# Performance work log

Measured on AMD Instinct MI355X. Metric: run time of the kernel, lower is better.

## Reference

```python
import jax, jax.numpy as jnp
import numpy as np

D_IN = 384
HID = 384
D_OUT = 384

def _kaiming(key, fan_in, fan_out):
    return jax.random.normal(key, (fan_in, fan_out), dtype=jnp.float32) * np.sqrt(2.0 / fan_in)

def setup_inputs() -> dict:
    key = jax.random.key(0)
    ks = jax.random.split(key, 12)
    B, O, T = 8, 1024, 8192
    obj_vecs = jax.random.normal(ks[0], (B, O, D_IN), dtype=jnp.float32)
    pred_vecs = jax.random.normal(ks[1], (B, T, D_IN), dtype=jnp.float32)
    edges = jax.random.randint(ks[2], (B, T, 2), 0, O, dtype=jnp.int64)
    # gconv1: [3D -> H -> 2H + Dout]; gconv2: [H -> H -> Dout]
    w1a = _kaiming(ks[3], 3 * D_IN, HID); b1a = jnp.zeros((HID,), jnp.float32)
    w1b = _kaiming(ks[4], HID, 2 * HID + D_OUT); b1b = jnp.zeros((2 * HID + D_OUT,), jnp.float32)
    w2a = _kaiming(ks[5], HID, HID); b2a = jnp.zeros((HID,), jnp.float32)
    w2b = _kaiming(ks[6], HID, D_OUT); b2b = jnp.zeros((D_OUT,), jnp.float32)
    return {"obj_vecs": obj_vecs, "pred_vecs": pred_vecs, "edges": edges,
            "w1a": w1a, "b1a": b1a, "w1b": w1b, "b1b": b1b,
            "w2a": w2a, "b2a": b2a, "w2b": w2b, "b2b": b2b}

def _gconv_forward(obj_vecs, pred_vecs, edges, w1a, b1a, w1b, b1b, w2a, b2a, w2b, b2b):
    B, O, D = obj_vecs.shape
    s_idx = edges[:, :, 0]  # (B, T)
    o_idx = edges[:, :, 1]
    batch = jnp.arange(B)[:, None]
    subj = obj_vecs[batch, s_idx]  # (B, T, D) gather
    objt = obj_vecs[batch, o_idx]
    triple = jnp.concatenate([subj, pred_vecs, objt], axis=-1)  # (B, T, 3D)
    h = jax.nn.relu(triple @ w1a + b1a)
    t = jax.nn.relu(h @ w1b + b1b)  # (B, T, 2H + Dout)
    new_s = t[:, :, :HID]
    new_p = t[:, :, HID:HID + D_OUT]
    new_o = t[:, :, HID + D_OUT:]
    # scatter_add per batch into (O, H) buffers
    def agg(si, oi, vs, vo):
        return jnp.zeros((O, HID), vs.dtype).at[si].add(vs).at[oi].add(vo)
    pooled = jax.vmap(agg)(s_idx, o_idx, new_s, new_o)  # (B, O, H)
    pooled = pooled / jnp.linalg.norm(pooled)  # global Frobenius norm, as in torch .norm()
    out_obj = jax.nn.relu(jax.nn.relu(pooled @ w2a + b2a) @ w2b + b2b)
    return out_obj, new_p

def reference(obj_vecs, pred_vecs, edges, w1a, b1a, w1b, b1b, w2a, b2a, w2b, b2b):
    return _gconv_forward(obj_vecs, pred_vecs, edges, w1a, b1a, w1b, b1b, w2a, b2a, w2b, b2b)
```

## Files before the change

kernel.cpp:

```cpp
#include <hip/hip_runtime.h>
#include <hip/hip_bf16.h>

#define NB 8
#define NT 8192
#define NO 1024
#define DD 384
#define K1 1152
#define M1 65536
#define MO 8192

typedef __attribute__((ext_vector_type(8))) short bf16x8;
typedef __attribute__((ext_vector_type(4))) float f32x4;
typedef __attribute__((ext_vector_type(4))) unsigned short u16x4;

__device__ __forceinline__ unsigned short f2bf(float f) {
    union { float f; unsigned u; } v; v.f = f;
    unsigned r = v.u + 0x7FFFu + ((v.u >> 16) & 1u);
    return (unsigned short)(r >> 16);
}
__device__ __forceinline__ float bf2f(unsigned short h) {
    union { unsigned u; float f; } v; v.u = ((unsigned)h) << 16;
    return v.f;
}
__device__ __forceinline__ bf16x8 pack8(f32x4 a, f32x4 b) {
    bf16x8 r;
    r[0] = (short)f2bf(a[0]); r[1] = (short)f2bf(a[1]);
    r[2] = (short)f2bf(a[2]); r[3] = (short)f2bf(a[3]);
    r[4] = (short)f2bf(b[0]); r[5] = (short)f2bf(b[1]);
    r[6] = (short)f2bf(b[2]); r[7] = (short)f2bf(b[3]);
    return r;
}
__device__ __forceinline__ void gload16(const void* g, void* l) {
    __builtin_amdgcn_global_load_lds(
        (const __attribute__((address_space(1))) unsigned int*)g,
        (__attribute__((address_space(3))) unsigned int*)l, 16, 0, 0);
}

__global__ void k_cvt4(const float* __restrict__ s, unsigned short* __restrict__ d, int n) {
    int i = (blockIdx.x * blockDim.x + threadIdx.x) * 4;
    if (i >= n) return;
    f32x4 v = *(const f32x4*)(s + i);
    u16x4 o;
    o[0] = f2bf(v[0]); o[1] = f2bf(v[1]); o[2] = f2bf(v[2]); o[3] = f2bf(v[3]);
    *(u16x4*)(d + i) = o;
}
__global__ void k_tr(const float* __restrict__ s, unsigned short* __restrict__ d, int K, int N) {
    int k = blockIdx.x;
    int n = blockIdx.y * blockDim.x + threadIdx.x;
    if (n < N) d[n * K + k] = f2bf(s[k * N + n]);
}

__global__ void k_ss1(const float* __restrict__ p, float* __restrict__ partial, int n4) {
    __shared__ float wsum[4];
    int stride = gridDim.x * blockDim.x;
    float s = 0.f;
    for (int i = blockIdx.x * blockDim.x + threadIdx.x; i < n4; i += stride) {
        f32x4 v = *(const f32x4*)(p + i * 4);
        s += v[0] * v[0] + v[1] * v[1] + v[2] * v[2] + v[3] * v[3];
    }
#pragma unroll
    for (int off = 32; off; off >>= 1) s += __shfl_down(s, off, 64);
    if ((threadIdx.x & 63) == 0) wsum[threadIdx.x >> 6] = s;
    __syncthreads();
    if (threadIdx.x == 0)
        partial[blockIdx.x] = wsum[0] + wsum[1] + wsum[2] + wsum[3];
}
__global__ void k_ss2(const float* __restrict__ partial, float* __restrict__ o) {
    float s = partial[threadIdx.x];
#pragma unroll
    for (int off = 32; off; off >>= 1) s += __shfl_down(s, off, 64);
    __shared__ float w0, w1;
    if (threadIdx.x == 0) w0 = s;
    if (threadIdx.x == 64) w1 = s;
    __syncthreads();
    if (threadIdx.x == 0) o[0] = w0 + w1;
}
__global__ void k_normcvt(const float* __restrict__ p, const float* __restrict__ ss,
                          unsigned short* __restrict__ o) {
    int i = (blockIdx.x * blockDim.x + threadIdx.x) * 8;
    float s = rsqrtf(ss[0]);
    f32x4 a = *(const f32x4*)(p + i), b = *(const f32x4*)(p + i + 4);
    a *= s; b *= s;
    *(bf16x8*)(o + i) = pack8(a, b);
}

__global__ void k_hist(const int* __restrict__ edges, int* __restrict__ cnt) {
    int i = blockIdx.x * 256 + threadIdx.x;
    int2 e = *(const int2*)&edges[(size_t)i * 2];
    int b = i >> 13;
    atomicAdd(&cnt[(b << 10) + e.x], 1);
    atomicAdd(&cnt[(b << 10) + e.y], 1);
}
__global__ void k_scan(const int* __restrict__ cnt, int* __restrict__ offs) {
    __shared__ int a[1024];
    int b = blockIdx.x, t = threadIdx.x;
    int own = cnt[(b << 10) + t];
    a[t] = own;
    __syncthreads();
    for (int s = 1; s < 1024; s <<= 1) {
        int v = (t >= s) ? a[t - s] : 0;
        __syncthreads();
        a[t] += v;
        __syncthreads();
    }
    offs[(b << 10) + t] = a[t] - own;
}
__global__ void k_fill(const int* __restrict__ edges, const int* __restrict__ offs,
                       int* __restrict__ cur, int* __restrict__ elist) {
    int i = blockIdx.x * 256 + threadIdx.x;
    int2 e = *(const int2*)&edges[(size_t)i * 2];
    int b = i >> 13, t = i & (NT - 1);
    int ps = atomicAdd(&cur[(b << 10) + e.x], 1);
    elist[(b << 14) + offs[(b << 10) + e.x] + ps] = t * 2;
    int po = atomicAdd(&cur[(b << 10) + e.y], 1);
    elist[(b << 14) + offs[(b << 10) + e.y] + po] = t * 2 + 1;
}
__global__ void k_pool(const unsigned short* __restrict__ sob, const int* __restrict__ cnt,
                       const int* __restrict__ offs, const int* __restrict__ elist,
                       float* __restrict__ pooled) {
    int w = (blockIdx.x * 256 + threadIdx.x) >> 6;
    int lane = threadIdx.x & 63;
    if (lane >= 48) return;
    int b = w >> 10, o = w & (NO - 1);
    int len = cnt[(b << 10) + o];
    const int* lst = elist + (b << 14) + offs[(b << 10) + o];
    f32x4 a0 = {0.f, 0.f, 0.f, 0.f}, a1 = {0.f, 0.f, 0.f, 0.f};
    f32x4 c0 = {0.f, 0.f, 0.f, 0.f}, c1 = {0.f, 0.f, 0.f, 0.f};
    int j = 0;
    for (; j + 1 < len; j += 2) {
        int e0 = lst[j], e1 = lst[j + 1];
        bf16x8 v0 = *(const bf16x8*)(sob + ((size_t)((b << 13) + (e0 >> 1))) * 768 + (e0 & 1) * DD + lane * 8);
        bf16x8 v1 = *(const bf16x8*)(sob + ((size_t)((b << 13) + (e1 >> 1))) * 768 + (e1 & 1) * DD + lane * 8);
        a0[0] += bf2f((unsigned short)v0[0]); a0[1] += bf2f((unsigned short)v0[1]);
        a0[2] += bf2f((unsigned short)v0[2]); a0[3] += bf2f((unsigned short)v0[3]);
        a1[0] += bf2f((unsigned short)v0[4]); a1[1] += bf2f((unsigned short)v0[5]);
        a1[2] += bf2f((unsigned short)v0[6]); a1[3] += bf2f((unsigned short)v0[7]);
        c0[0] += bf2f((unsigned short)v1[0]); c0[1] += bf2f((unsigned short)v1[1]);
        c0[2] += bf2f((unsigned short)v1[2]); c0[3] += bf2f((unsigned short)v1[3]);
        c1[0] += bf2f((unsigned short)v1[4]); c1[1] += bf2f((unsigned short)v1[5]);
        c1[2] += bf2f((unsigned short)v1[6]); c1[3] += bf2f((unsigned short)v1[7]);
    }
    if (j < len) {
        int e0 = lst[j];
        bf16x8 v0 = *(const bf16x8*)(sob + ((size_t)((b << 13) + (e0 >> 1))) * 768 + (e0 & 1) * DD + lane * 8);
        a0[0] += bf2f((unsigned short)v0[0]); a0[1] += bf2f((unsigned short)v0[1]);
        a0[2] += bf2f((unsigned short)v0[2]); a0[3] += bf2f((unsigned short)v0[3]);
        a1[0] += bf2f((unsigned short)v0[4]); a1[1] += bf2f((unsigned short)v0[5]);
        a1[2] += bf2f((unsigned short)v0[6]); a1[3] += bf2f((unsigned short)v0[7]);
    }
    a0 += c0; a1 += c1;
    float* dst = pooled + ((size_t)((b << 10) + o)) * DD + lane * 8;
    *(f32x4*)dst = a0;
    *(f32x4*)(dst + 4) = a1;
}

__launch_bounds__(512, 1)
__global__ void gemm_g1(const unsigned short* __restrict__ objb,
                        const float* __restrict__ predf,
                        const int* __restrict__ edges,
                        const unsigned short* __restrict__ Bt,
                        const float* __restrict__ bias,
                        unsigned short* __restrict__ outb)
{
    const int tid = threadIdx.x;
    const int lane = tid & 63;
    const int d = blockIdx.x;
    const int bid = (d & 7) * 64 + (d >> 3);
    const int m0 = bid * 128;

    __shared__ unsigned short lds[2][32768];

    const int rb = tid >> 3;
    const int c8 = ((tid & 7) ^ (rb & 7)) * 8;

    const int bb = (m0 >> 13) << 10;
    int er0[2], er1[2];
#pragma unroll
    for (int i = 0; i < 2; ++i) {
        int2 e = *(const int2*)&edges[(size_t)(m0 + i * 64 + rb) * 2];
        er0[i] = bb + e.x;
        er1[i] = bb + e.y;
    }

    f32x4 acc[4][6];
#pragma unroll
    for (int i = 0; i < 4; ++i)
#pragma unroll
        for (int j = 0; j < 6; ++j) acc[i][j] = (f32x4){0.f, 0.f, 0.f, 0.f};

    const int wid = tid >> 6, wm = wid >> 2, wn = wid & 3;
    const int l16 = lane & 15, lg = lane >> 4;

#pragma unroll
    for (int i = 0; i < 2; ++i)
        gload16(objb + (size_t)er0[i] * DD + c8, &lds[0][i * 4096 + tid * 8]);
#pragma unroll
    for (int i = 0; i < 6; ++i)
        gload16(Bt + (size_t)(i * 64 + rb) * K1 + c8, &lds[0][8192 + i * 4096 + tid * 8]);

    const int nsteps = K1 / 64;
    for (int t = 0; t < nsteps; ++t) {
        const int cur = t & 1;
        const int tn = t + 1;
        if (tn < nsteps) {
            const int nseg = tn / 6;
            const int ko = (tn - nseg * 6) * 64;
            if (nseg == 1) {
                f32x4 pf[2][2];
#pragma unroll
                for (int i = 0; i < 2; ++i) {
                    const float* p = predf + (size_t)(m0 + i * 64 + rb) * DD + ko + c8;
                    pf[i][0] = *(const f32x4*)p;
                    pf[i][1] = *(const f32x4*)(p + 4);
                }
#pragma unroll
                for (int i = 0; i < 6; ++i)
                    gload16(Bt + (size_t)(i * 64 + rb) * K1 + tn * 64 + c8,
                            &lds[cur ^ 1][8192 + i * 4096 + tid * 8]);
#pragma unroll
                for (int i = 0; i < 2; ++i)
                    *(bf16x8*)(&lds[cur ^ 1][i * 4096 + tid * 8]) = pack8(pf[i][0], pf[i][1]);
            } else {
                const unsigned short* asrc0 = (nseg == 0) ? objb + (size_t)er0[0] * DD + ko + c8
                                                          : objb + (size_t)er1[0] * DD + ko + c8;
                const unsigned short* asrc1 = (nseg == 0) ? objb + (size_t)er0[1] * DD + ko + c8
                                                          : objb + (size_t)er1[1] * DD + ko + c8;
                gload16(asrc0, &lds[cur ^ 1][0 * 4096 + tid * 8]);
                gload16(asrc1, &lds[cur ^ 1][1 * 4096 + tid * 8]);
#pragma unroll
                for (int i = 0; i < 6; ++i)
                    gload16(Bt + (size_t)(i * 64 + rb) * K1 + tn * 64 + c8,
                            &lds[cur ^ 1][8192 + i * 4096 + tid * 8]);
                asm volatile("s_waitcnt vmcnt(8)" ::: "memory");
            }
        } else {
            asm volatile("s_waitcnt vmcnt(0)" ::: "memory");
        }
        __builtin_amdgcn_s_barrier();
        const unsigned short* At = &lds[cur][0];
        const unsigned short* Bl = &lds[cur][8192];
#pragma unroll
        for (int kt = 0; kt < 2; ++kt) {
            const int cs = ((kt * 4 + lg) ^ (l16 & 7)) * 8;
            bf16x8 af[4], bfr[6];
#pragma unroll
            for (int mt = 0; mt < 4; ++mt)
                af[mt] = *(const bf16x8*)(At + (wm * 64 + mt * 16 + l16) * 64 + cs);
#pragma unroll
            for (int nn = 0; nn < 6; ++nn)
                bfr[nn] = *(const bf16x8*)(Bl + (wn * 96 + nn * 16 + l16) * 64 + cs);
#pragma unroll
            for (int mt = 0; mt < 4; ++mt)
#pragma unroll
                for (int nn = 0; nn < 6; ++nn)
                    acc[mt][nn] = __builtin_amdgcn_mfma_f32_16x16x32_bf16(af[mt], bfr[nn], acc[mt][nn], 0, 0, 0);
        }
        asm volatile("s_waitcnt lgkmcnt(0)" ::: "memory");
        __builtin_amdgcn_s_barrier();
    }

#pragma unroll
    for (int nn = 0; nn < 6; ++nn) {
        int gn = wn * 96 + nn * 16 + l16;
        float bv = bias[gn];
#pragma unroll
        for (int mt = 0; mt < 4; ++mt) {
            int rbase = wm * 64 + mt * 16 + lg * 4;
#pragma unroll
            for (int rg = 0; rg < 4; ++rg) {
                int gr = m0 + rbase + rg;
                float v = fmaxf(acc[mt][nn][rg] + bv, 0.0f);
                outb[(size_t)gr * DD + gn] = f2bf(v);
            }
        }
    }
}

template <int EPI, int YFOLD>
__launch_bounds__(512, 1)
__global__ void gemm_p(const unsigned short* __restrict__ Abf,
                       const unsigned short* __restrict__ Bt,
                       const float* __restrict__ bias,
                       unsigned short* __restrict__ outb,
                       float* __restrict__ outf,
                       int K, int ldC, int bt0p, int btys, int cstride)
{
    const int tid = threadIdx.x;
    const int lane = tid & 63;
    const int d = blockIdx.x;
    const int chunk = gridDim.x >> 3;
    const int bid = (d & 7) * chunk + (d >> 3);
    int xb, y;
    if (YFOLD) { y = bid & 1; xb = bid >> 1; }
    else       { y = 0;       xb = bid;      }
    const int m0 = xb * 128;
    const int bt0 = bt0p + y * btys;
    const int col0 = y * cstride;

    __shared__ unsigned short lds[2][32768];

    const int rb = tid >> 3;
    const int c8 = ((tid & 7) ^ (rb & 7)) * 8;

    f32x4 acc[4][6];
#pragma unroll
    for (int i = 0; i < 4; ++i)
#pragma unroll
        for (int j = 0; j < 6; ++j) acc[i][j] = (f32x4){0.f, 0.f, 0.f, 0.f};

    const int wid = tid >> 6, wm = wid >> 2, wn = wid & 3;
    const int l16 = lane & 15, lg = lane >> 4;

#define STAGE_P(BUF, KK)                                                                   \
    {                                                                                      \
        _Pragma("unroll")                                                                  \
        for (int i = 0; i < 6; ++i)                                                        \
            gload16(Bt + (size_t)(bt0 + i * 64 + rb) * K + (KK) + c8,                      \
                    &lds[BUF][8192 + i * 4096 + tid * 8]);                                 \
        _Pragma("unroll")                                                                  \
        for (int i = 0; i < 2; ++i)                                                        \
            gload16(Abf + (size_t)(m0 + i * 64 + rb) * K + (KK) + c8,                      \
                    &lds[BUF][i * 4096 + tid * 8]);                                        \
    }

    const int nt = K / 64;
    STAGE_P(0, 0)
    for (int t = 0; t < nt; ++t) {
        const int cur = t & 1;
        if (t + 1 < nt) {
            STAGE_P(cur ^ 1, (t + 1) * 64)
            asm volatile("s_waitcnt vmcnt(8)" ::: "memory");
        } else {
            asm volatile("s_waitcnt vmcnt(0)" ::: "memory");
        }
        __builtin_amdgcn_s_barrier();
        const unsigned short* At = &lds[cur][0];
        const unsigned short* Bl = &lds[cur][8192];
#pragma unroll
        for (int kt = 0; kt < 2; ++kt) {
            const int cs = ((kt * 4 + lg) ^ (l16 & 7)) * 8;
            bf16x8 af[4], bfr[6];
#pragma unroll
            for (int mt = 0; mt < 4; ++mt)
                af[mt] = *(const bf16x8*)(At + (wm * 64 + mt * 16 + l16) * 64 + cs);
#pragma unroll
            for (int nn = 0; nn < 6; ++nn)
                bfr[nn] = *(const bf16x8*)(Bl + (wn * 96 + nn * 16 + l16) * 64 + cs);
#pragma unroll
            for (int mt = 0; mt < 4; ++mt)
#pragma unroll
                for (int nn = 0; nn < 6; ++nn)
                    acc[mt][nn] = __builtin_amdgcn_mfma_f32_16x16x32_bf16(af[mt], bfr[nn], acc[mt][nn], 0, 0, 0);
        }
        asm volatile("s_waitcnt lgkmcnt(0)" ::: "memory");
        __builtin_amdgcn_s_barrier();
    }
#undef STAGE_P

#pragma unroll
    for (int nn = 0; nn < 6; ++nn) {
        int gn = wn * 96 + nn * 16 + l16;
        float bv = bias[bt0 + gn];
#pragma unroll
        for (int mt = 0; mt < 4; ++mt) {
            int rbase = wm * 64 + mt * 16 + lg * 4;
#pragma unroll
            for (int rg = 0; rg < 4; ++rg) {
                int gr = m0 + rbase + rg;
                float v = fmaxf(acc[mt][nn][rg] + bv, 0.0f);
                if (EPI == 0) outb[(size_t)gr * ldC + col0 + gn] = f2bf(v);
                else          outf[(size_t)gr * ldC + col0 + gn] = v;
            }
        }
    }
}

extern "C" void kernel_launch(void* const* d_in, const int* in_sizes, int n_in,
                              void* d_out, int out_size, void* d_ws, size_t ws_size,
                              hipStream_t stream)
{
    const float* obj  = (const float*)d_in[0];
    const float* pred = (const float*)d_in[1];
    const int* edges  = (const int*)d_in[2];
    const float* w1a  = (const float*)d_in[3];
    const float* b1a  = (const float*)d_in[4];
    const float* w1b  = (const float*)d_in[5];
    const float* b1b  = (const float*)d_in[6];
    const float* w2a  = (const float*)d_in[7];
    const float* b2a  = (const float*)d_in[8];
    const float* w2b  = (const float*)d_in[9];
    const float* b2b  = (const float*)d_in[10];

    float* out_obj = (float*)d_out;
    float* newp    = out_obj + (size_t)MO * DD;
    unsigned short* sob = (unsigned short*)newp;

    unsigned short* objb = (unsigned short*)d_ws;
    unsigned short* w1aT = objb + (size_t)NB * NO * DD;
    unsigned short* w1bT = w1aT + (size_t)DD * K1;
    unsigned short* w2aT = w1bT + (size_t)K1 * DD;
    unsigned short* w2bT = w2aT + (size_t)DD * DD;
    unsigned short* hbuf = w2bT + (size_t)DD * DD;
    float* pooled = (float*)(hbuf + (size_t)M1 * DD);
    float* sumsq  = pooled + (size_t)MO * DD;
    unsigned short* hid2 = (unsigned short*)(sumsq + 4);
    int* cnt   = (int*)(hid2 + (size_t)MO * DD);
    int* cur   = cnt + NB * NO;
    int* offs  = cur + NB * NO;
    int* elist = offs + NB * NO;
    float* partial = (float*)(elist + 2 * M1);
    unsigned short* poolb = objb;

    hipLaunchKernelGGL(k_cvt4, dim3(3072), dim3(256), 0, stream, obj, objb, NB * NO * DD);
    hipLaunchKernelGGL(k_tr, dim3(K1, 3), dim3(128), 0, stream, w1a, w1aT, K1, DD);
    hipLaunchKernelGGL(k_tr, dim3(DD, 9), dim3(128), 0, stream, w1b, w1bT, DD, K1);
    hipLaunchKernelGGL(k_tr, dim3(DD, 3), dim3(128), 0, stream, w2a, w2aT, DD, DD);
    hipLaunchKernelGGL(k_tr, dim3(DD, 3), dim3(128), 0, stream, w2b, w2bT, DD, DD);
    hipMemsetAsync(cnt, 0, 2 * NB * NO * sizeof(int), stream);

    hipLaunchKernelGGL(gemm_g1, dim3(M1 / 128), dim3(512), 0, stream,
                       objb, pred, edges, w1aT, b1a, hbuf);

    hipLaunchKernelGGL((gemm_p<0, 1>), dim3(2 * M1 / 128), dim3(512), 0, stream,
                       hbuf, w1bT, b1b, sob, (float*)nullptr, DD, 2 * DD, 0, 2 * DD, DD);

    hipLaunchKernelGGL(k_hist, dim3(256), dim3(256), 0, stream, edges, cnt);
    hipLaunchKernelGGL(k_scan, dim3(8), dim3(1024), 0, stream, cnt, offs);
    hipLaunchKernelGGL(k_fill, dim3(256), dim3(256), 0, stream, edges, offs, cur, elist);
    hipLaunchKernelGGL(k_pool, dim3(2048), dim3(256), 0, stream, sob, cnt, offs, elist, pooled);

    hipLaunchKernelGGL((gemm_p<2, 0>), dim3(M1 / 128), dim3(512), 0, stream,
                       hbuf, w1bT, b1b, (unsigned short*)nullptr, newp, DD, DD, DD, 0, 0);

    hipLaunchKernelGGL(k_ss1, dim3(128), dim3(256), 0, stream, pooled, partial, MO * DD / 4);
    hipLaunchKernelGGL(k_ss2, dim3(1), dim3(128), 0, stream, partial, sumsq);
    hipLaunchKernelGGL(k_normcvt, dim3(1536), dim3(256), 0, stream, pooled, sumsq, poolb);

    hipLaunchKernelGGL((gemm_p<0, 0>), dim3(MO / 128), dim3(512), 0, stream,
                       poolb, w2aT, b2a, hid2, (float*)nullptr, DD, DD, 0, 0, 0);

    hipLaunchKernelGGL((gemm_p<2, 0>), dim3(MO / 128), dim3(512), 0, stream,
                       hid2, w2bT, b2b, (unsigned short*)nullptr, out_obj, DD, DD, 0, 0, 0);
}
```

Measured before the change: 270.0 us.

## Pre-pack GEMM operands into tiled swizzled images for contiguous LDS loads

Weights and intermediate activations (hidden buffer, normalized pooled, hid2) are written directly in a per-k-tile, per-row-block swizzled image layout that matches the LDS layout. Each GEMM stage can then fetch a fully contiguous 64 KB chunk per tile with global_load_lds instead of strided row loads. Producer epilogues now do scattered 2-byte stores into the image layout, and the weight packing kernel reads with strided access.

Result: slower. 302.6 us (+12.1%).

```diff
diff --git a/kernel.cpp b/kernel.cpp
--- a/kernel.cpp
+++ b/kernel.cpp
@@ -35,6 +35,10 @@
         (const __attribute__((address_space(1))) unsigned int*)g,
         (__attribute__((address_space(3))) unsigned int*)l, 16, 0, 0);
 }
+__device__ __forceinline__ size_t aimg_off(int kt, int nblk, int blk, int r, int kc) {
+    return ((size_t)(kt * nblk + blk)) * 8192 + (size_t)((r >> 6) * 4096)
+         + (size_t)(((r & 63) * 8 + ((kc >> 3) ^ (r & 7))) * 8) + (kc & 7);
+}
 
 __global__ void k_cvt4(const float* __restrict__ s, unsigned short* __restrict__ d, int n) {
     int i = (blockIdx.x * blockDim.x + threadIdx.x) * 4;
@@ -44,10 +48,23 @@
     o[0] = f2bf(v[0]); o[1] = f2bf(v[1]); o[2] = f2bf(v[2]); o[3] = f2bf(v[3]);
     *(u16x4*)(d + i) = o;
 }
-__global__ void k_tr(const float* __restrict__ s, unsigned short* __restrict__ d, int K, int N) {
-    int k = blockIdx.x;
-    int n = blockIdx.y * blockDim.x + threadIdx.x;
-    if (n < N) d[n * K + k] = f2bf(s[k * N + n]);
+__global__ void k_pack(const float* __restrict__ src, unsigned short* __restrict__ dst,
+                       int Nsrc, int ntiles) {
+    const int tid = threadIdx.x;
+    const int kt = blockIdx.x, panel = blockIdx.y;
+    const int rb = tid >> 3;
+    const int c8 = ((tid & 7) ^ (rb & 7)) * 8;
+    const int base_row = panel * 384;
+    unsigned short* d = dst + ((size_t)(panel * ntiles + kt)) * 24576 + tid * 8;
+#pragma unroll
+    for (int i = 0; i < 6; ++i) {
+        int row = base_row + i * 64 + rb;
+        bf16x8 v;
+#pragma unroll
+        for (int j = 0; j < 8; ++j)
+            v[j] = (short)f2bf(src[(size_t)(kt * 64 + c8 + j) * Nsrc + row]);
+        *(bf16x8*)(d + i * 4096) = v;
+    }
 }
 
 __global__ void k_ss1(const float* __restrict__ p, float* __restrict__ partial, int n4) {
@@ -76,12 +93,14 @@
     if (threadIdx.x == 0) o[0] = w0 + w1;
 }
 __global__ void k_normcvt(const float* __restrict__ p, const float* __restrict__ ss,
-                          unsigned short* __restrict__ o) {
-    int i = (blockIdx.x * blockDim.x + threadIdx.x) * 8;
+                          unsigned short* __restrict__ oimg) {
+    int u = blockIdx.x * 256 + threadIdx.x;
+    int m = u / 48, k0 = (u - m * 48) * 8;
     float s = rsqrtf(ss[0]);
-    f32x4 a = *(const f32x4*)(p + i), b = *(const f32x4*)(p + i + 4);
+    f32x4 a = *(const f32x4*)(p + (size_t)m * DD + k0);
+    f32x4 b = *(const f32x4*)(p + (size_t)m * DD + k0 + 4);
     a *= s; b *= s;
-    *(bf16x8*)(o + i) = pack8(a, b);
+    *(bf16x8*)(oimg + aimg_off(k0 >> 6, 64, m >> 7, m & 127, k0 & 63)) = pack8(a, b);
 }
 
 __global__ void k_hist(const int* __restrict__ edges, int* __restrict__ cnt) {
@@ -158,9 +177,9 @@
 __global__ void gemm_g1(const unsigned short* __restrict__ objb,
                         const float* __restrict__ predf,
                         const int* __restrict__ edges,
-                        const unsigned short* __restrict__ Bt,
+                        const unsigned short* __restrict__ Bimg,
                         const float* __restrict__ bias,
-                        unsigned short* __restrict__ outb)
+                        unsigned short* __restrict__ outimg)
 {
     const int tid = threadIdx.x;
     const int lane = tid & 63;
@@ -196,7 +215,7 @@
         gload16(objb + (size_t)er0[i] * DD + c8, &lds[0][i * 4096 + tid * 8]);
 #pragma unroll
     for (int i = 0; i < 6; ++i)
-        gload16(Bt + (size_t)(i * 64 + rb) * K1 + c8, &lds[0][8192 + i * 4096 + tid * 8]);
+        gload16(Bimg + i * 4096 + tid * 8, &lds[0][8192 + i * 4096 + tid * 8]);
 
     const int nsteps = K1 / 64;
     for (int t = 0; t < nsteps; ++t) {
@@ -215,7 +234,7 @@
                 }
 #pragma unroll
                 for (int i = 0; i < 6; ++i)
-                    gload16(Bt + (size_t)(i * 64 + rb) * K1 + tn * 64 + c8,
+                    gload16(Bimg + (size_t)tn * 24576 + i * 4096 + tid * 8,
                             &lds[cur ^ 1][8192 + i * 4096 + tid * 8]);
 #pragma unroll
                 for (int i = 0; i < 2; ++i)
@@ -229,7 +248,7 @@
                 gload16(asrc1, &lds[cur ^ 1][1 * 4096 + tid * 8]);
 #pragma unroll
                 for (int i = 0; i < 6; ++i)
-                    gload16(Bt + (size_t)(i * 64 + rb) * K1 + tn * 64 + c8,
+                    gload16(Bimg + (size_t)tn * 24576 + i * 4096 + tid * 8,
                             &lds[cur ^ 1][8192 + i * 4096 + tid * 8]);
                 asm volatile("s_waitcnt vmcnt(8)" ::: "memory");
             }
@@ -270,7 +289,7 @@
             for (int rg = 0; rg < 4; ++rg) {
                 int gr = m0 + rbase + rg;
                 float v = fmaxf(acc[mt][nn][rg] + bv, 0.0f);
-                outb[(size_t)gr * DD + gn] = f2bf(v);
+                outimg[aimg_off(gn >> 6, 512, gr >> 7, gr & 127, gn & 63)] = f2bf(v);
             }
         }
     }
@@ -278,12 +297,13 @@
 
 template <int EPI, int YFOLD>
 __launch_bounds__(512, 1)
-__global__ void gemm_p(const unsigned short* __restrict__ Abf,
-                       const unsigned short* __restrict__ Bt,
+__global__ void gemm_p(const unsigned short* __restrict__ Aimg,
+                       const unsigned short* __restrict__ Bimg,
                        const float* __restrict__ bias,
                        unsigned short* __restrict__ outb,
                        float* __restrict__ outf,
-                       int K, int ldC, int bt0p, int btys, int cstride)
+                       int ntile, int anblk, int onblk, int ldC,
+                       int bt0p, int btys, int cstride, int bimg_y_off)
 {
     const int tid = threadIdx.x;
     const int lane = tid & 63;
@@ -296,11 +316,9 @@
     const int m0 = xb * 128;
     const int bt0 = bt0p + y * btys;
     const int col0 = y * cstride;
+    const unsigned short* Bp = Bimg + (size_t)y * bimg_y_off;
 
     __shared__ unsigned short lds[2][32768];
-
-    const int rb = tid >> 3;
-    const int c8 = ((tid & 7) ^ (rb & 7)) * 8;
 
     f32x4 acc[4][6];
 #pragma unroll
@@ -311,24 +329,23 @@
     const int wid = tid >> 6, wm = wid >> 2, wn = wid & 3;
     const int l16 = lane & 15, lg = lane >> 4;
 
-#define STAGE_P(BUF, KK)                                                                   \
+#define STAGE_P(BUF, T)                                                                    \
     {                                                                                      \
         _Pragma("unroll")                                                                  \
         for (int i = 0; i < 6; ++i)                                                        \
-            gload16(Bt + (size_t)(bt0 + i * 64 + rb) * K + (KK) + c8,                      \
+            gload16(Bp + (size_t)(T) * 24576 + i * 4096 + tid * 8,                         \
                     &lds[BUF][8192 + i * 4096 + tid * 8]);                                 \
         _Pragma("unroll")                                                                  \
         for (int i = 0; i < 2; ++i)                                                        \
-            gload16(Abf + (size_t)(m0 + i * 64 + rb) * K + (KK) + c8,                      \
+            gload16(Aimg + ((size_t)((T) * anblk + xb)) * 8192 + i * 4096 + tid * 8,       \
                     &lds[BUF][i * 4096 + tid * 8]);                                        \
     }
 
-    const int nt = K / 64;
     STAGE_P(0, 0)
-    for (int t = 0; t < nt; ++t) {
+    for (int t = 0; t < ntile; ++t) {
         const int cur = t & 1;
-        if (t + 1 < nt) {
-            STAGE_P(cur ^ 1, (t + 1) * 64)
+        if (t + 1 < ntile) {
+            STAGE_P(cur ^ 1, t + 1)
             asm volatile("s_waitcnt vmcnt(8)" ::: "memory");
         } else {
             asm volatile("s_waitcnt vmcnt(0)" ::: "memory");
@@ -368,8 +385,9 @@
             for (int rg = 0; rg < 4; ++rg) {
                 int gr = m0 + rbase + rg;
                 float v = fmaxf(acc[mt][nn][rg] + bv, 0.0f);
-                if (EPI == 0) outb[(size_t)gr * ldC + col0 + gn] = f2bf(v);
-                else          outf[(size_t)gr * ldC + col0 + gn] = v;
+                if (EPI == 0)      outb[(size_t)gr * ldC + col0 + gn] = f2bf(v);
+                else if (EPI == 2) outf[(size_t)gr * ldC + col0 + gn] = v;
+                else               outb[aimg_off(gn >> 6, onblk, gr >> 7, gr & 127, gn & 63)] = f2bf(v);
             }
         }
     }
@@ -395,34 +413,35 @@
     float* newp    = out_obj + (size_t)MO * DD;
     unsigned short* sob = (unsigned short*)newp;
 
-    unsigned short* objb = (unsigned short*)d_ws;
-    unsigned short* w1aT = objb + (size_t)NB * NO * DD;
-    unsigned short* w1bT = w1aT + (size_t)DD * K1;
-    unsigned short* w2aT = w1bT + (size_t)K1 * DD;
-    unsigned short* w2bT = w2aT + (size_t)DD * DD;
-    unsigned short* hbuf = w2bT + (size_t)DD * DD;
-    float* pooled = (float*)(hbuf + (size_t)M1 * DD);
+    unsigned short* objb   = (unsigned short*)d_ws;
+    unsigned short* w1aImg = objb + (size_t)NB * NO * DD;
+    unsigned short* w1bImg = w1aImg + (size_t)18 * 24576;
+    unsigned short* w2aImg = w1bImg + (size_t)18 * 24576;
+    unsigned short* w2bImg = w2aImg + (size_t)6 * 24576;
+    unsigned short* hbufImg = w2bImg + (size_t)6 * 24576;
+    float* pooled = (float*)(hbufImg + (size_t)6 * 512 * 8192);
     float* sumsq  = pooled + (size_t)MO * DD;
-    unsigned short* hid2 = (unsigned short*)(sumsq + 4);
-    int* cnt   = (int*)(hid2 + (size_t)MO * DD);
+    unsigned short* hid2Img = (unsigned short*)(sumsq + 4);
+    int* cnt   = (int*)(hid2Img + (size_t)6 * 64 * 8192);
     int* cur   = cnt + NB * NO;
     int* offs  = cur + NB * NO;
     int* elist = offs + NB * NO;
     float* partial = (float*)(elist + 2 * M1);
-    unsigned short* poolb = objb;
+    unsigned short* poolbImg = objb;
 
     hipLaunchKernelGGL(k_cvt4, dim3(3072), dim3(256), 0, stream, obj, objb, NB * NO * DD);
-    hipLaunchKernelGGL(k_tr, dim3(K1, 3), dim3(128), 0, stream, w1a, w1aT, K1, DD);
-    hipLaunchKernelGGL(k_tr, dim3(DD, 9), dim3(128), 0, stream, w1b, w1bT, DD, K1);
-    hipLaunchKernelGGL(k_tr, dim3(DD, 3), dim3(128), 0, stream, w2a, w2aT, DD, DD);
-    hipLaunchKernelGGL(k_tr, dim3(DD, 3), dim3(128), 0, stream, w2b, w2bT, DD, DD);
+    hipLaunchKernelGGL(k_pack, dim3(18, 1), dim3(512), 0, stream, w1a, w1aImg, DD, 18);
+    hipLaunchKernelGGL(k_pack, dim3(6, 3), dim3(512), 0, stream, w1b, w1bImg, K1, 6);
+    hipLaunchKernelGGL(k_pack, dim3(6, 1), dim3(512), 0, stream, w2a, w2aImg, DD, 6);
+    hipLaunchKernelGGL(k_pack, dim3(6, 1), dim3(512), 0, stream, w2b, w2bImg, DD, 6);
     hipMemsetAsync(cnt, 0, 2 * NB * NO * sizeof(int), stream);
 
     hipLaunchKernelGGL(gemm_g1, dim3(M1 / 128), dim3(512), 0, stream,
-                       objb, pred, edges, w1aT, b1a, hbuf);
+                       objb, pred, edges, w1aImg, b1a, hbufImg);
 
     hipLaunchKernelGGL((gemm_p<0, 1>), dim3(2 * M1 / 128), dim3(512), 0, stream,
-                       hbuf, w1bT, b1b, sob, (float*)nullptr, DD, 2 * DD, 0, 2 * DD, DD);
+                       hbufImg, w1bImg, b1b, sob, (float*)nullptr,
+                       6, 512, 0, 2 * DD, 0, 2 * DD, DD, 2 * 6 * 24576);
 
     hipLaunchKernelGGL(k_hist, dim3(256), dim3(256), 0, stream, edges, cnt);
     hipLaunchKernelGGL(k_scan, dim3(8), dim3(1024), 0, stream, cnt, offs);
@@ -430,15 +449,18 @@
     hipLaunchKernelGGL(k_pool, dim3(2048), dim3(256), 0, stream, sob, cnt, offs, elist, pooled);
 
     hipLaunchKernelGGL((gemm_p<2, 0>), dim3(M1 / 128), dim3(512), 0, stream,
-                       hbuf, w1bT, b1b, (unsigned short*)nullptr, newp, DD, DD, DD, 0, 0);
+                       hbufImg, w1bImg + (size_t)6 * 24576, b1b, (unsigned short*)nullptr, newp,
+                       6, 512, 0, DD, DD, 0, 0, 0);
 
     hipLaunchKernelGGL(k_ss1, dim3(128), dim3(256), 0, stream, pooled, partial, MO * DD / 4);
     hipLaunchKernelGGL(k_ss2, dim3(1), dim3(128), 0, stream, partial, sumsq);
-    hipLaunchKernelGGL(k_normcvt, dim3(1536), dim3(256), 0, stream, pooled, sumsq, poolb);
-
-    hipLaunchKernelGGL((gemm_p<0, 0>), dim3(MO / 128), dim3(512), 0, stream,
-                       poolb, w2aT, b2a, hid2, (float*)nullptr, DD, DD, 0, 0, 0);
+    hipLaunchKernelGGL(k_normcvt, dim3(1536), dim3(256), 0, stream, pooled, sumsq, poolbImg);
+
+    hipLaunchKernelGGL((gemm_p<3, 0>), dim3(MO / 128), dim3(512), 0, stream,
+                       poolbImg, w2aImg, b2a, hid2Img, (float*)nullptr,
+                       6, 64, 64, 0, 0, 0, 0, 0);
 
     hipLaunchKernelGGL((gemm_p<2, 0>), dim3(MO / 128), dim3(512), 0, stream,
-                       hid2, w2bT, b2b, (unsigned short*)nullptr, out_obj, DD, DD, 0, 0, 0);
-}
+                       hid2Img, w2bImg, b2b, (unsigned short*)nullptr, out_obj,
+                       6, 64, 0, DD, 0, 0, 0, 0);
+}
```

## Shrink GEMM tiles to 128x128 with 256-thread blocks for more occupancy

Applied to the files above, without the earlier changes.

All GEMM kernels move from 128x384 tiles and 512-thread blocks to 128x128 tiles and 256-thread blocks, with two blocks per CU. The grid gains an N-block dimension, and column offsets into the fused w1b weight are remapped through new nbn/osplit/oadd parameters. This gives more blocks and better load balance, and lets two blocks overlap memory latency on each CU. In exchange, the A operand (including the gathered object rows and the pred conversion) is reloaded once per N-block, which raises global traffic.

New measurement: 256.7 us. 4.9% less time.

```diff
diff --git a/kernel.cpp b/kernel.cpp
--- a/kernel.cpp
+++ b/kernel.cpp
@@ -154,7 +154,7 @@
     *(f32x4*)(dst + 4) = a1;
 }
 
-__launch_bounds__(512, 1)
+__launch_bounds__(256, 2)
 __global__ void gemm_g1(const unsigned short* __restrict__ objb,
                         const float* __restrict__ predf,
                         const int* __restrict__ edges,
@@ -165,38 +165,41 @@
     const int tid = threadIdx.x;
     const int lane = tid & 63;
     const int d = blockIdx.x;
-    const int bid = (d & 7) * 64 + (d >> 3);
-    const int m0 = bid * 128;
-
-    __shared__ unsigned short lds[2][32768];
+    const int chunk = gridDim.x >> 3;
+    const int bid = (d & 7) * chunk + (d >> 3);
+    const int xb = bid / 3, nb = bid - xb * 3;
+    const int m0 = xb * 128;
+    const int btrow = nb * 128;
+
+    __shared__ unsigned short lds[2][16384];
 
     const int rb = tid >> 3;
     const int c8 = ((tid & 7) ^ (rb & 7)) * 8;
 
     const int bb = (m0 >> 13) << 10;
-    int er0[2], er1[2];
-#pragma unroll
-    for (int i = 0; i < 2; ++i) {
-        int2 e = *(const int2*)&edges[(size_t)(m0 + i * 64 + rb) * 2];
+    int er0[4], er1[4];
+#pragma unroll
+    for (int i = 0; i < 4; ++i) {
+        int2 e = *(const int2*)&edges[(size_t)(m0 + i * 32 + rb) * 2];
         er0[i] = bb + e.x;
         er1[i] = bb + e.y;
     }
 
-    f32x4 acc[4][6];
+    f32x4 acc[4][4];
 #pragma unroll
     for (int i = 0; i < 4; ++i)
 #pragma unroll
-        for (int j = 0; j < 6; ++j) acc[i][j] = (f32x4){0.f, 0.f, 0.f, 0.f};
-
-    const int wid = tid >> 6, wm = wid >> 2, wn = wid & 3;
+        for (int j = 0; j < 4; ++j) acc[i][j] = (f32x4){0.f, 0.f, 0.f, 0.f};
+
+    const int wid = tid >> 6, wm = wid >> 1, wn = wid & 1;
     const int l16 = lane & 15, lg = lane >> 4;
 
 #pragma unroll
-    for (int i = 0; i < 2; ++i)
-        gload16(objb + (size_t)er0[i] * DD + c8, &lds[0][i * 4096 + tid * 8]);
-#pragma unroll
-    for (int i = 0; i < 6; ++i)
-        gload16(Bt + (size_t)(i * 64 + rb) * K1 + c8, &lds[0][8192 + i * 4096 + tid * 8]);
+    for (int i = 0; i < 4; ++i)
+        gload16(objb + (size_t)er0[i] * DD + c8, &lds[0][i * 2048 + tid * 8]);
+#pragma unroll
+    for (int i = 0; i < 4; ++i)
+        gload16(Bt + (size_t)(btrow + i * 32 + rb) * K1 + c8, &lds[0][8192 + i * 2048 + tid * 8]);
 
     const int nsteps = K1 / 64;
     for (int t = 0; t < nsteps; ++t) {
@@ -206,31 +209,30 @@
             const int nseg = tn / 6;
             const int ko = (tn - nseg * 6) * 64;
             if (nseg == 1) {
-                f32x4 pf[2][2];
-#pragma unroll
-                for (int i = 0; i < 2; ++i) {
-                    const float* p = predf + (size_t)(m0 + i * 64 + rb) * DD + ko + c8;
+                f32x4 pf[4][2];
+#pragma unroll
+                for (int i = 0; i < 4; ++i) {
+                    const float* p = predf + (size_t)(m0 + i * 32 + rb) * DD + ko + c8;
                     pf[i][0] = *(const f32x4*)p;
                     pf[i][1] = *(const f32x4*)(p + 4);
                 }
 #pragma unroll
-                for (int i = 0; i < 6; ++i)
-                    gload16(Bt + (size_t)(i * 64 + rb) * K1 + tn * 64 + c8,
-                            &lds[cur ^ 1][8192 + i * 4096 + tid * 8]);
-#pragma unroll
-                for (int i = 0; i < 2; ++i)
-                    *(bf16x8*)(&lds[cur ^ 1][i * 4096 + tid * 8]) = pack8(pf[i][0], pf[i][1]);
+                for (int i = 0; i < 4; ++i)
+                    gload16(Bt + (size_t)(btrow + i * 32 + rb) * K1 + tn * 64 + c8,
+                            &lds[cur ^ 1][8192 + i * 2048 + tid * 8]);
+#pragma unroll
+                for (int i = 0; i < 4; ++i)
+                    *(bf16x8*)(&lds[cur ^ 1][i * 2048 + tid * 8]) = pack8(pf[i][0], pf[i][1]);
             } else {
-                const unsigned short* asrc0 = (nseg == 0) ? objb + (size_t)er0[0] * DD + ko + c8
-                                                          : objb + (size_t)er1[0] * DD + ko + c8;
-                const unsigned short* asrc1 = (nseg == 0) ? objb + (size_t)er0[1] * DD + ko + c8
-                                                          : objb + (size_t)er1[1] * DD + ko + c8;
-                gload16(asrc0, &lds[cur ^ 1][0 * 4096 + tid * 8]);
-                gload16(asrc1, &lds[cur ^ 1][1 * 4096 + tid * 8]);
-#pragma unroll
-                for (int i = 0; i < 6; ++i)
-                    gload16(Bt + (size_t)(i * 64 + rb) * K1 + tn * 64 + c8,
-                            &lds[cur ^ 1][8192 + i * 4096 + tid * 8]);
+#pragma unroll
+                for (int i = 0; i < 4; ++i) {
+                    int row = (nseg == 0) ? er0[i] : er1[i];
+                    gload16(objb + (size_t)row * DD + ko + c8, &lds[cur ^ 1][i * 2048 + tid * 8]);
+                }
+#pragma unroll
+                for (int i = 0; i < 4; ++i)
+                    gload16(Bt + (size_t)(btrow + i * 32 + rb) * K1 + tn * 64 + c8,
+                            &lds[cur ^ 1][8192 + i * 2048 + tid * 8]);
                 asm volatile("s_waitcnt vmcnt(8)" ::: "memory");
             }
         } else {
@@ -242,17 +244,17 @@
 #pragma unroll
         for (int kt = 0; kt < 2; ++kt) {
             const int cs = ((kt * 4 + lg) ^ (l16 & 7)) * 8;
-            bf16x8 af[4], bfr[6];
+            bf16x8 af[4], bfr[4];
 #pragma unroll
             for (int mt = 0; mt < 4; ++mt)
                 af[mt] = *(const bf16x8*)(At + (wm * 64 + mt * 16 + l16) * 64 + cs);
 #pragma unroll
-            for (int nn = 0; nn < 6; ++nn)
-                bfr[nn] = *(const bf16x8*)(Bl + (wn * 96 + nn * 16 + l16) * 64 + cs);
+            for (int nn = 0; nn < 4; ++nn)
+                bfr[nn] = *(const bf16x8*)(Bl + (wn * 64 + nn * 16 + l16) * 64 + cs);
 #pragma unroll
             for (int mt = 0; mt < 4; ++mt)
 #pragma unroll
-                for (int nn = 0; nn < 6; ++nn)
+                for (int nn = 0; nn < 4; ++nn)
                     acc[mt][nn] = __builtin_amdgcn_mfma_f32_16x16x32_bf16(af[mt], bfr[nn], acc[mt][nn], 0, 0, 0);
         }
         asm volatile("s_waitcnt lgkmcnt(0)" ::: "memory");
@@ -260,8 +262,8 @@
     }
 
 #pragma unroll
-    for (int nn = 0; nn < 6; ++nn) {
-        int gn = wn * 96 + nn * 16 + l16;
+    for (int nn = 0; nn < 4; ++nn) {
+        int gn = btrow + wn * 64 + nn * 16 + l16;
         float bv = bias[gn];
 #pragma unroll
         for (int mt = 0; mt < 4; ++mt) {
@@ -276,51 +278,49 @@
     }
 }
 
-template <int EPI, int YFOLD>
-__launch_bounds__(512, 1)
+template <int EPI>
+__launch_bounds__(256, 2)
 __global__ void gemm_p(const unsigned short* __restrict__ Abf,
                        const unsigned short* __restrict__ Bt,
                        const float* __restrict__ bias,
                        unsigned short* __restrict__ outb,
                        float* __restrict__ outf,
-                       int K, int ldC, int bt0p, int btys, int cstride)
+                       int K, int ldC, int nbn, int osplit, int oadd)
 {
     const int tid = threadIdx.x;
     const int lane = tid & 63;
     const int d = blockIdx.x;
     const int chunk = gridDim.x >> 3;
     const int bid = (d & 7) * chunk + (d >> 3);
-    int xb, y;
-    if (YFOLD) { y = bid & 1; xb = bid >> 1; }
-    else       { y = 0;       xb = bid;      }
+    const int xb = bid / nbn, nb = bid - xb * nbn;
     const int m0 = xb * 128;
-    const int bt0 = bt0p + y * btys;
-    const int col0 = y * cstride;
-
-    __shared__ unsigned short lds[2][32768];
+    const int btrow = nb * 128 + (nb >= osplit ? oadd : 0);
+    const int col0 = nb * 128;
+
+    __shared__ unsigned short lds[2][16384];
 
     const int rb = tid >> 3;
     const int c8 = ((tid & 7) ^ (rb & 7)) * 8;
 
-    f32x4 acc[4][6];
+    f32x4 acc[4][4];
 #pragma unroll
     for (int i = 0; i < 4; ++i)
 #pragma unroll
-        for (int j = 0; j < 6; ++j) acc[i][j] = (f32x4){0.f, 0.f, 0.f, 0.f};
-
-    const int wid = tid >> 6, wm = wid >> 2, wn = wid & 3;
+        for (int j = 0; j < 4; ++j) acc[i][j] = (f32x4){0.f, 0.f, 0.f, 0.f};
+
+    const int wid = tid >> 6, wm = wid >> 1, wn = wid & 1;
     const int l16 = lane & 15, lg = lane >> 4;
 
 #define STAGE_P(BUF, KK)                                                                   \
     {                                                                                      \
         _Pragma("unroll")                                                                  \
-        for (int i = 0; i < 6; ++i)                                                        \
-            gload16(Bt + (size_t)(bt0 + i * 64 + rb) * K + (KK) + c8,                      \
-                    &lds[BUF][8192 + i * 4096 + tid * 8]);                                 \
+        for (int i = 0; i < 4; ++i)                                                        \
+            gload16(Bt + (size_t)(btrow + i * 32 + rb) * K + (KK) + c8,                    \
+                    &lds[BUF][8192 + i * 2048 + tid * 8]);                                 \
         _Pragma("unroll")                                                                  \
-        for (int i = 0; i < 2; ++i)                                                        \
-            gload16(Abf + (size_t)(m0 + i * 64 + rb) * K + (KK) + c8,                      \
-                    &lds[BUF][i * 4096 + tid * 8]);                                        \
+        for (int i = 0; i < 4; ++i)                                                        \
+            gload16(Abf + (size_t)(m0 + i * 32 + rb) * K + (KK) + c8,                      \
+                    &lds[BUF][i * 2048 + tid * 8]);                                        \
     }
 
     const int nt = K / 64;
@@ -339,17 +339,17 @@
 #pragma unroll
         for (int kt = 0; kt < 2; ++kt) {
             const int cs = ((kt * 4 + lg) ^ (l16 & 7)) * 8;
-            bf16x8 af[4], bfr[6];
+            bf16x8 af[4], bfr[4];
 #pragma unroll
             for (int mt = 0; mt < 4; ++mt)
                 af[mt] = *(const bf16x8*)(At + (wm * 64 + mt * 16 + l16) * 64 + cs);
 #pragma unroll
-            for (int nn = 0; nn < 6; ++nn)
-                bfr[nn] = *(const bf16x8*)(Bl + (wn * 96 + nn * 16 + l16) * 64 + cs);
+            for (int nn = 0; nn < 4; ++nn)
+                bfr[nn] = *(const bf16x8*)(Bl + (wn * 64 + nn * 16 + l16) * 64 + cs);
 #pragma unroll
             for (int mt = 0; mt < 4; ++mt)
 #pragma unroll
-                for (int nn = 0; nn < 6; ++nn)
+                for (int nn = 0; nn < 4; ++nn)
                     acc[mt][nn] = __builtin_amdgcn_mfma_f32_16x16x32_bf16(af[mt], bfr[nn], acc[mt][nn], 0, 0, 0);
         }
         asm volatile("s_waitcnt lgkmcnt(0)" ::: "memory");
@@ -358,9 +358,9 @@
 #undef STAGE_P
 
 #pragma unroll
-    for (int nn = 0; nn < 6; ++nn) {
-        int gn = wn * 96 + nn * 16 + l16;
-        float bv = bias[bt0 + gn];
+    for (int nn = 0; nn < 4; ++nn) {
+        int gnl = wn * 64 + nn * 16 + l16;
+        float bv = bias[btrow + gnl];
 #pragma unroll
         for (int mt = 0; mt < 4; ++mt) {
             int rbase = wm * 64 + mt * 16 + lg * 4;
@@ -368,8 +368,8 @@
             for (int rg = 0; rg < 4; ++rg) {
                 int gr = m0 + rbase + rg;
                 float v = fmaxf(acc[mt][nn][rg] + bv, 0.0f);
-                if (EPI == 0) outb[(size_t)gr * ldC + col0 + gn] = f2bf(v);
-                else          outf[(size_t)gr * ldC + col0 + gn] = v;
+                if (EPI == 0) outb[(size_t)gr * ldC + col0 + gnl] = f2bf(v);
+                else          outf[(size_t)gr * ldC + col0 + gnl] = v;
             }
         }
     }
@@ -418,27 +418,27 @@
     hipLaunchKernelGGL(k_tr, dim3(DD, 3), dim3(128), 0, stream, w2b, w2bT, DD, DD);
     hipMemsetAsync(cnt, 0, 2 * NB * NO * sizeof(int), stream);
 
-    hipLaunchKernelGGL(gemm_g1, dim3(M1 / 128), dim3(512), 0, stream,
+    hipLaunchKernelGGL(gemm_g1, dim3(3 * M1 / 128), dim3(256), 0, stream,
                        objb, pred, edges, w1aT, b1a, hbuf);
 
-    hipLaunchKernelGGL((gemm_p<0, 1>), dim3(2 * M1 / 128), dim3(512), 0, stream,
-                       hbuf, w1bT, b1b, sob, (float*)nullptr, DD, 2 * DD, 0, 2 * DD, DD);
+    hipLaunchKernelGGL((gemm_p<0>), dim3(6 * M1 / 128), dim3(256), 0, stream,
+                       hbuf, w1bT, b1b, sob, (float*)nullptr, DD, 2 * DD, 6, 3, DD);
 
     hipLaunchKernelGGL(k_hist, dim3(256), dim3(256), 0, stream, edges, cnt);
     hipLaunchKernelGGL(k_scan, dim3(8), dim3(1024), 0, stream, cnt, offs);
     hipLaunchKernelGGL(k_fill, dim3(256), dim3(256), 0, stream, edges, offs, cur, elist);
     hipLaunchKernelGGL(k_pool, dim3(2048), dim3(256), 0, stream, sob, cnt, offs, elist, pooled);
 
-    hipLaunchKernelGGL((gemm_p<2, 0>), dim3(M1 / 128), dim3(512), 0, stream,
-                       hbuf, w1bT, b1b, (unsigned short*)nullptr, newp, DD, DD, DD, 0, 0);
+    hipLaunchKernelGGL((gemm_p<2>), dim3(3 * M1 / 128), dim3(256), 0, stream,
+                       hbuf, w1bT, b1b, (unsigned short*)nullptr, newp, DD, DD, 3, 0, DD);
 
     hipLaunchKernelGGL(k_ss1, dim3(128), dim3(256), 0, stream, pooled, partial, MO * DD / 4);
     hipLaunchKernelGGL(k_ss2, dim3(1), dim3(128), 0, stream, partial, sumsq);
     hipLaunchKernelGGL(k_normcvt, dim3(1536), dim3(256), 0, stream, pooled, sumsq, poolb);
 
-    hipLaunchKernelGGL((gemm_p<0, 0>), dim3(MO / 128), dim3(512), 0, stream,
-                       poolb, w2aT, b2a, hid2, (float*)nullptr, DD, DD, 0, 0, 0);
-
-    hipLaunchKernelGGL((gemm_p<2, 0>), dim3(MO / 128), dim3(512), 0, stream,
-                       hid2, w2bT, b2b, (unsigned short*)nullptr, out_obj, DD, DD, 0, 0, 0);
-}
+    hipLaunchKernelGGL((gemm_p<0>), dim3(3 * MO / 128), dim3(256), 0, stream,
+                       poolb, w2aT, b2a, hid2, (float*)nullptr, DD, DD, 3, 3, 0);
+
+    hipLaunchKernelGGL((gemm_p<2>), dim3(3 * MO / 128), dim3(256), 0, stream,
+                       hid2, w2bT, b2b, (unsigned short*)nullptr, out_obj, DD, DD, 3, 3, 0);
+}
```
